# Optimization experiments

Measured on AMD Instinct MI355X. Metric: run time of the kernel, lower is better.

## Reference

```python
import jax, jax.numpy as jnp
import numpy as np

B, S = 1024, 64          # batch, num clips (att_size)
R = 1024                 # CG_rnn_size
E = 1024                 # CG_input_encoding_size
CD = 1024                # clip_context_dim
ED = 1024                # event_context_dim
H = 512                  # CG_att_hid_size


def setup_inputs() -> dict:
    key = jax.random.key(0)
    ks = jax.random.split(key, 20)
    s = 0.02
    return {
        "xt": jax.random.normal(ks[0], (B, E), jnp.float32),
        "video": jax.random.normal(ks[1], (B, 1024), jnp.float32),
        "event": jax.random.normal(ks[2], (B, ED), jnp.float32),
        "clip": jax.random.normal(ks[3], (B, S, CD), jnp.float32),
        "clip_mask": jax.random.randint(ks[4], (B, S), 0, 2, jnp.int32),
        "state_h": jax.random.normal(ks[5], (2, B, R), jnp.float32),
        "state_c": jax.random.normal(ks[6], (2, B, R), jnp.float32),
        # LSTMCell 0 (input = event ++ xt -> ED+E)
        "W_ih0": jax.random.normal(ks[7], (4 * R, ED + E), jnp.float32) * s,
        "b_ih0": jnp.zeros((4 * R,), jnp.float32),
        "W_hh0": jax.random.normal(ks[8], (4 * R, R), jnp.float32) * s,
        "b_hh0": jnp.zeros((4 * R,), jnp.float32),
        # LSTMCell 1 (input = att ++ xt -> CD+E)
        "W_ih1": jax.random.normal(ks[9], (4 * R, CD + E), jnp.float32) * s,
        "b_ih1": jnp.zeros((4 * R,), jnp.float32),
        "W_hh1": jax.random.normal(ks[10], (4 * R, R), jnp.float32) * s,
        "b_hh1": jnp.zeros((4 * R,), jnp.float32),
        # Attention params
        "W_ctx": jax.random.normal(ks[11], (H, CD), jnp.float32) * s,
        "b_ctx": jnp.zeros((H,), jnp.float32),
        "W_h2a": jax.random.normal(ks[12], (H, R), jnp.float32) * s,
        "b_h2a": jnp.zeros((H,), jnp.float32),
        "W_alpha": jax.random.normal(ks[13], (1, H), jnp.float32) * s,
        "b_alpha": jnp.zeros((1,), jnp.float32),
    }


def _lstm_cell(x, h, c, W_ih, b_ih, W_hh, b_hh):
    gates = x @ W_ih.T + b_ih + h @ W_hh.T + b_hh  # [B, 4R]
    i, f, g, o = jnp.split(gates, 4, axis=-1)
    i, f, o = jax.nn.sigmoid(i), jax.nn.sigmoid(f), jax.nn.sigmoid(o)
    g = jnp.tanh(g)
    c_new = f * c + i * g
    h_new = o * jnp.tanh(c_new)
    return h_new, c_new


def _attention(h, att_feats, att_mask, W_ctx, b_ctx, W_h2a, b_h2a, W_alpha, b_alpha):
    att = att_feats @ W_ctx.T + b_ctx                 # [B, S, H]
    att_h = h @ W_h2a.T + b_h2a                       # [B, H]
    dot = jnp.tanh(att + att_h[:, None, :])           # [B, S, H]
    scores = (dot @ W_alpha.T + b_alpha)[..., 0]      # [B, S]
    weight = jax.nn.softmax(scores, axis=1)
    m = att_mask.astype(weight.dtype)
    weight = weight * m
    weight = weight / jnp.sum(weight, axis=1, keepdims=True)
    return jnp.einsum('bs,bsd->bd', weight, att_feats)  # [B, CD]


def reference(xt, video, event, clip, clip_mask, state_h, state_c,
              W_ih0, b_ih0, W_hh0, b_hh0, W_ih1, b_ih1, W_hh1, b_hh1,
              W_ctx, b_ctx, W_h2a, b_h2a, W_alpha, b_alpha):
    pre_h1 = state_h[1]
    # stream 0: torch.cat((xt, event), 1)
    h0, c0 = _lstm_cell(jnp.concatenate([xt, event], axis=1),
                        state_h[0], state_c[0], W_ih0, b_ih0, W_hh0, b_hh0)
    att = _attention(pre_h1, clip, clip_mask,
                     W_ctx, b_ctx, W_h2a, b_h2a, W_alpha, b_alpha)
    h1, c1 = _lstm_cell(jnp.concatenate([xt, att], axis=1),
                        state_h[1], state_c[1], W_ih1, b_ih1, W_hh1, b_hh1)
    # dropout layers are identity in eval mode
    output = jnp.concatenate([h0, h1], axis=1)        # [B, 2R]
    new_h = jnp.stack([h0, h1])
    new_c = jnp.stack([c0, c1])
    return output, new_h, new_c
```

## Files before the change

kernel.cpp:

```cpp
#include <hip/hip_runtime.h>

typedef short short8 __attribute__((ext_vector_type(8)));
typedef float floatx4 __attribute__((ext_vector_type(4)));
typedef unsigned short u16;

__device__ __forceinline__ u16 cvt_bf(float x) {
  unsigned u = __float_as_uint(x);
  unsigned r = 0x7FFFu + ((u >> 16) & 1u);
  return (u16)((u + r) >> 16);
}
__device__ __forceinline__ float bf2f(u16 h) {
  return __uint_as_float(((unsigned)h) << 16);
}
__device__ __forceinline__ void gll16(const u16* g, u16* l) {
  __builtin_amdgcn_global_load_lds(
      (__attribute__((address_space(1))) void*)(void*)const_cast<u16*>(g),
      (__attribute__((address_space(3))) void*)(void*)l, 16, 0, 0);
}
__device__ __forceinline__ float fast_tanh(float x) {
  float t = __expf(-2.f * fabsf(x));
  float r = 1.f - 2.f * t / (1.f + t);
  return copysignf(r, x);
}
__device__ __forceinline__ float fast_sigm(float x) {
  return 1.f / (1.f + __expf(-x));
}

#define MAXSEG 9
struct ConvArgs {
  const float* src[MAXSEG];
  u16* dst[MAXSEG];
  unsigned lw[MAXSEG];
  unsigned dstride[MAXSEG];
  unsigned blk0[MAXSEG + 1];
  int nseg;
};
__global__ __launch_bounds__(256)
void convert_seg(ConvArgs a) {
  const unsigned blk = blockIdx.x;
  int s = 0;
  for (int i = 1; i < a.nseg; ++i) if (blk >= a.blk0[i]) s = i;
  const unsigned e0 = (blk - a.blk0[s]) * 2048u + threadIdx.x * 8u;
  const float* src = a.src[s] + e0;
  const float4 v0 = *(const float4*)src;
  const float4 v1 = *(const float4*)(src + 4);
  const unsigned row = e0 >> a.lw[s];
  const unsigned col = e0 & ((1u << a.lw[s]) - 1u);
  u16* d = a.dst[s] + (size_t)row * a.dstride[s] + col;
  short8 p;
  p[0] = (short)cvt_bf(v0.x); p[1] = (short)cvt_bf(v0.y);
  p[2] = (short)cvt_bf(v0.z); p[3] = (short)cvt_bf(v0.w);
  p[4] = (short)cvt_bf(v1.x); p[5] = (short)cvt_bf(v1.y);
  p[6] = (short)cvt_bf(v1.z); p[7] = (short)cvt_bf(v1.w);
  *(short8*)d = p;
}
__global__ __launch_bounds__(256)
void conv_flat(const float* __restrict__ src, u16* __restrict__ dst) {
  const size_t e = (size_t)blockIdx.x * 2048 + threadIdx.x * 8;
  const float4 v0 = *(const float4*)(src + e);
  const float4 v1 = *(const float4*)(src + e + 4);
  short8 p;
  p[0] = (short)cvt_bf(v0.x); p[1] = (short)cvt_bf(v0.y);
  p[2] = (short)cvt_bf(v0.z); p[3] = (short)cvt_bf(v0.w);
  p[4] = (short)cvt_bf(v1.x); p[5] = (short)cvt_bf(v1.y);
  p[6] = (short)cvt_bf(v1.z); p[7] = (short)cvt_bf(v1.w);
  *(short8*)(dst + e) = p;
}
__global__ __launch_bounds__(256)
void zerof(float* __restrict__ p) { p[blockIdx.x * 256 + threadIdx.x] = 0.f; }

template<int MODE>
__global__ __launch_bounds__(256, 3)
void gemm128(const u16* __restrict__ A, int sa, const u16* __restrict__ B, int sb,
             const float* __restrict__ bias0, const float* __restrict__ bias1,
             float* __restrict__ out, int N, int K,
             const float* __restrict__ atth, const float* __restrict__ Walpha,
             float* __restrict__ scores, int row0,
             const u16* A2, const u16* B2,
             const float* bias0b, const float* bias1b, float* out2)
{
  if (blockIdx.z) { A = A2; B = B2; bias0 = bias0b; bias1 = bias1b; out = out2; }
  __shared__ u16 sA[128 * 64];
  __shared__ u16 sB[128 * 64];

  const int tid = threadIdx.x, lane = tid & 63, w = tid >> 6;
  const int quad = lane >> 4, l15 = lane & 15;
  const int wm = w >> 1, wn = w & 1;
  const int Mbase = blockIdx.y * 128, Nbase = blockIdx.x * 128;
  const int srow = lane >> 3;
  const int sslot = (lane & 7) ^ srow;

  floatx4 acc[4][4] = {};

  for (int k0 = 0; k0 < K; k0 += 64) {
    __syncthreads();
#pragma unroll
    for (int j = 0; j < 4; ++j) {
      const int c = w + 4 * j;
      const int row = c * 8 + srow;
      gll16(A + (size_t)(Mbase + row) * sa + k0 + sslot * 8, &sA[c * 512]);
      gll16(B + (size_t)(Nbase + row) * sb + k0 + sslot * 8, &sB[c * 512]);
    }
    __syncthreads();
#pragma unroll
    for (int ks = 0; ks < 2; ++ks) {
      short8 af[4], bf[4];
#pragma unroll
      for (int mt = 0; mt < 4; ++mt) {
        const int row = wm * 64 + mt * 16 + l15;
        af[mt] = *(const short8*)&sA[row * 64 + ((ks * 4 + quad) ^ (row & 7)) * 8];
      }
#pragma unroll
      for (int nt = 0; nt < 4; ++nt) {
        const int row = wn * 64 + nt * 16 + l15;
        bf[nt] = *(const short8*)&sB[row * 64 + ((ks * 4 + quad) ^ (row & 7)) * 8];
      }
#pragma unroll
      for (int mt = 0; mt < 4; ++mt)
#pragma unroll
        for (int nt = 0; nt < 4; ++nt)
          acc[mt][nt] = __builtin_amdgcn_mfma_f32_16x16x32_bf16(af[mt], bf[nt], acc[mt][nt], 0, 0, 0);
    }
  }

  if (MODE == 0) {
#pragma unroll
    for (int nt = 0; nt < 4; ++nt) {
      const int col = Nbase + wn * 64 + nt * 16 + l15;
      const float bc = bias0[col] + bias1[col];
#pragma unroll
      for (int mt = 0; mt < 4; ++mt) {
        const int rb = Mbase + wm * 64 + mt * 16 + quad * 4;
#pragma unroll
        for (int r = 0; r < 4; ++r)
          out[(size_t)(rb + r) * N + col] = acc[mt][nt][r] + bc;
      }
    }
  } else {
    const int b = (row0 + Mbase + wm * 64) >> 6;
    float rs[4][4] = {};
#pragma unroll
    for (int nt = 0; nt < 4; ++nt) {
      const int col = Nbase + wn * 64 + nt * 16 + l15;
      const float wa = Walpha[col];
      const float ah = atth[(size_t)b * 512 + col];
#pragma unroll
      for (int mt = 0; mt < 4; ++mt)
#pragma unroll
        for (int r = 0; r < 4; ++r)
          rs[mt][r] += wa * fast_tanh(acc[mt][nt][r] + ah);
    }
#pragma unroll
    for (int mt = 0; mt < 4; ++mt)
#pragma unroll
      for (int r = 0; r < 4; ++r) {
        float v = rs[mt][r];
        v += __shfl_xor(v, 1); v += __shfl_xor(v, 2);
        v += __shfl_xor(v, 4); v += __shfl_xor(v, 8);
        if (l15 == 0)
          atomicAdd(&scores[row0 + Mbase + wm * 64 + mt * 16 + quad * 4 + r], v);
      }
  }
}

__global__ __launch_bounds__(256)
void softmax_k(const float* __restrict__ scores, const int* __restrict__ mask,
               float* __restrict__ wbuf)
{
  const int b = blockIdx.x * 4 + (threadIdx.x >> 6);
  const int s = threadIdx.x & 63;
  const float v = scores[b * 64 + s];
  float mx = v;
#pragma unroll
  for (int d = 32; d; d >>= 1) mx = fmaxf(mx, __shfl_xor(mx, d));
  const float e = __expf(v - mx) * (float)mask[b * 64 + s];
  float den = e;
#pragma unroll
  for (int d = 32; d; d >>= 1) den += __shfl_xor(den, d);
  wbuf[b * 64 + s] = e / den;
}

template<int BF>
__global__ __launch_bounds__(128)
void ctx_att(const float* __restrict__ clipf, const u16* __restrict__ clipb,
             const float* __restrict__ wbuf, u16* __restrict__ A1)
{
  __shared__ float w[64];
  const int b = blockIdx.x, tid = threadIdx.x;
  if (tid < 64) w[tid] = wbuf[b * 64 + tid];
  __syncthreads();
  const int c8 = tid * 8;
  float a[8] = {};
  if (BF) {
    const u16* base = clipb + (size_t)b * 65536 + c8;
#pragma unroll 4
    for (int s = 0; s < 64; ++s) {
      const float wt = w[s];
      const short8 c = *(const short8*)(base + (size_t)s * 1024);
#pragma unroll
      for (int j = 0; j < 8; ++j) a[j] += wt * bf2f((u16)c[j]);
    }
  } else {
    const float* base = clipf + (size_t)b * 65536 + c8;
#pragma unroll 4
    for (int s = 0; s < 64; ++s) {
      const float wt = w[s];
      const float4 v0 = *(const float4*)(base + (size_t)s * 1024);
      const float4 v1 = *(const float4*)(base + (size_t)s * 1024 + 4);
      a[0] += wt * v0.x; a[1] += wt * v0.y; a[2] += wt * v0.z; a[3] += wt * v0.w;
      a[4] += wt * v1.x; a[5] += wt * v1.y; a[6] += wt * v1.z; a[7] += wt * v1.w;
    }
  }
  short8 p;
#pragma unroll
  for (int j = 0; j < 8; ++j) p[j] = (short)cvt_bf(a[j]);
  *(short8*)&A1[(size_t)b * 3072 + 1024 + c8] = p;
}

__global__ __launch_bounds__(256)
void lstm_ew(const float* __restrict__ gates, const float* __restrict__ cprev,
             float* __restrict__ out, int st)
{
  const int idx = blockIdx.x * 256 + threadIdx.x;
  const int b = idx >> 8;
  const int r4 = (idx & 255) * 4;
  const float* g = gates + (size_t)b * 4096 + r4;
  const float4 gi = *(const float4*)g;
  const float4 gf = *(const float4*)(g + 1024);
  const float4 gg = *(const float4*)(g + 2048);
  const float4 go = *(const float4*)(g + 3072);
  const float4 c  = *(const float4*)(cprev + (size_t)b * 1024 + r4);
  float4 cn, hn;
  cn.x = fast_sigm(gf.x) * c.x + fast_sigm(gi.x) * fast_tanh(gg.x);  hn.x = fast_sigm(go.x) * fast_tanh(cn.x);
  cn.y = fast_sigm(gf.y) * c.y + fast_sigm(gi.y) * fast_tanh(gg.y);  hn.y = fast_sigm(go.y) * fast_tanh(cn.y);
  cn.z = fast_sigm(gf.z) * c.z + fast_sigm(gi.z) * fast_tanh(gg.z);  hn.z = fast_sigm(go.z) * fast_tanh(cn.z);
  cn.w = fast_sigm(gf.w) * c.w + fast_sigm(gi.w) * fast_tanh(gg.w);  hn.w = fast_sigm(go.w) * fast_tanh(cn.w);
  *(float4*)(out + (size_t)b * 2048 + st * 1024 + r4) = hn;
  *(float4*)(out + 2097152 + (size_t)st * 1048576 + (size_t)b * 1024 + r4) = hn;
  *(float4*)(out + 4194304 + (size_t)st * 1048576 + (size_t)b * 1024 + r4) = cn;
}

extern "C" void kernel_launch(void* const* d_in, const int* in_sizes, int n_in,
                              void* d_out, int out_size, void* d_ws, size_t ws_size,
                              hipStream_t stream) {
  (void)in_sizes; (void)n_in; (void)out_size;
  const float* xt      = (const float*)d_in[0];
  const float* event   = (const float*)d_in[2];
  const float* clip    = (const float*)d_in[3];
  const int*   cmask   = (const int*)d_in[4];
  const float* state_h = (const float*)d_in[5];
  const float* state_c = (const float*)d_in[6];
  const float* W_ih0   = (const float*)d_in[7];
  const float* b_ih0   = (const float*)d_in[8];
  const float* W_hh0   = (const float*)d_in[9];
  const float* b_hh0   = (const float*)d_in[10];
  const float* W_ih1   = (const float*)d_in[11];
  const float* b_ih1   = (const float*)d_in[12];
  const float* W_hh1   = (const float*)d_in[13];
  const float* b_hh1   = (const float*)d_in[14];
  const float* W_ctx   = (const float*)d_in[15];
  const float* b_ctx   = (const float*)d_in[16];
  const float* W_h2a   = (const float*)d_in[17];
  const float* b_h2a   = (const float*)d_in[18];
  const float* W_alpha = (const float*)d_in[19];

  int NC; bool grouped;
  if      (ws_size >= 207618048) { NC = 1; grouped = true;  }
  else if (ws_size >= 106954752) { NC = 4; grouped = true;  }
  else                           { NC = 8; grouped = false; }

  char* p = (char*)d_ws;
  float* gates0 = (float*)p; p += 16777216;
  float* gates1 = gates0;
  if (grouped) { gates1 = (float*)p; p += 16777216; }
  u16* A0 = (u16*)p; p += 6291456;
  u16* A1 = (u16*)p; p += 6291456;
  u16* W0 = (u16*)p; p += 25165824;
  u16* Wc = (u16*)p; p += 1048576;
  u16* Wh = (u16*)p; p += 1048576;
  u16* clipb = (u16*)p;
  u16* W1 = (u16*)p;
  float* atth   = gates0;
  float* wbuf   = gates0 + 524288;
  float* scores = gates0 + 589824;

  const float* h0p = state_h;
  const float* h1p = state_h + 1048576;
  const float* c0p = state_c;
  const float* c1p = state_c + 1048576;
  float* out = (float*)d_out;

  ConvArgs ca{};
  {
    const float* srcs[9] = {W_ctx, W_h2a, W_ih0, W_hh0, xt, event, h0p, xt, h1p};
    u16* dsts[9] = {Wc, Wh, W0, W0 + 2048, A0, A0 + 1024, A0 + 2048, A1, A1 + 2048};
    const unsigned lws[9]  = {10, 10, 11, 10, 10, 10, 10, 10, 10};
    const unsigned dstr[9] = {1024, 1024, 3072, 3072, 3072, 3072, 3072, 3072, 3072};
    const unsigned nblk[9] = {256, 256, 4096, 2048, 512, 512, 512, 512, 512};
    unsigned acc = 0;
    for (int i = 0; i < 9; ++i) {
      ca.src[i] = srcs[i]; ca.dst[i] = dsts[i];
      ca.lw[i] = lws[i]; ca.dstride[i] = dstr[i];
      ca.blk0[i] = acc; acc += nblk[i];
    }
    ca.blk0[9] = acc; ca.nseg = 9;
    convert_seg<<<acc, 256, 0, stream>>>(ca);
  }

  zerof<<<256, 256, 0, stream>>>(scores);

  gemm128<0><<<dim3(4, 8, 1), 256, 0, stream>>>(
      A1 + 2048, 3072, Wh, 1024, b_h2a, b_ctx, atth, 512, 1024,
      nullptr, nullptr, nullptr, 0, nullptr, nullptr, nullptr, nullptr, nullptr);

  const int rows = 65536 / NC;
  for (int c = 0; c < NC; ++c) {
    conv_flat<<<rows * 1024 / 2048, 256, 0, stream>>>(clip + (size_t)c * rows * 1024, clipb);
    gemm128<1><<<dim3(4, rows / 128, 1), 256, 0, stream>>>(
        clipb, 1024, Wc, 1024, nullptr, nullptr, nullptr, 512, 1024,
        atth, W_alpha, scores, c * rows,
        nullptr, nullptr, nullptr, nullptr, nullptr);
  }

  softmax_k<<<256, 256, 0, stream>>>(scores, cmask, wbuf);

  if (NC == 1) ctx_att<1><<<1024, 128, 0, stream>>>(clip, clipb, wbuf, A1);
  else         ctx_att<0><<<1024, 128, 0, stream>>>(clip, clipb, wbuf, A1);

  ConvArgs cb{};
  {
    const float* srcs[2] = {W_ih1, W_hh1};
    u16* dsts[2] = {W1, W1 + 2048};
    const unsigned lws[2] = {11, 10};
    const unsigned nblk[2] = {4096, 2048};
    unsigned acc = 0;
    for (int i = 0; i < 2; ++i) {
      cb.src[i] = srcs[i]; cb.dst[i] = dsts[i];
      cb.lw[i] = lws[i]; cb.dstride[i] = 3072;
      cb.blk0[i] = acc; acc += nblk[i];
    }
    cb.blk0[2] = acc; cb.nseg = 2;
    convert_seg<<<acc, 256, 0, stream>>>(cb);
  }

  if (grouped) {
    gemm128<0><<<dim3(32, 8, 2), 256, 0, stream>>>(
        A0, 3072, W0, 3072, b_ih0, b_hh0, gates0, 4096, 3072,
        nullptr, nullptr, nullptr, 0,
        A1, W1, b_ih1, b_hh1, gates1);
    lstm_ew<<<1024, 256, 0, stream>>>(gates0, c0p, out, 0);
    lstm_ew<<<1024, 256, 0, stream>>>(gates1, c1p, out, 1);
  } else {
    gemm128<0><<<dim3(32, 8, 1), 256, 0, stream>>>(
        A0, 3072, W0, 3072, b_ih0, b_hh0, gates0, 4096, 3072,
        nullptr, nullptr, nullptr, 0, nullptr, nullptr, nullptr, nullptr, nullptr);
    lstm_ew<<<1024, 256, 0, stream>>>(gates0, c0p, out, 0);
    gemm128<0><<<dim3(32, 8, 1), 256, 0, stream>>>(
        A1, 3072, W1, 3072, b_ih1, b_hh1, gates0, 4096, 3072,
        nullptr, nullptr, nullptr, 0, nullptr, nullptr, nullptr, nullptr, nullptr);
    lstm_ew<<<1024, 256, 0, stream>>>(gates0, c1p, out, 1);
  }
}
```

Before: 710.4 us.

## Add large-workspace path fusing GEMMs and elementwise stages into fewer launches

With enough workspace, a new path converts all weights and the full clip tensor to bf16 at once. It then fuses independent work into shared launches: the h2a GEMM runs alongside the clip conversion, the LSTM0 GEMM alongside the attention-score GEMM, and the LSTM1 GEMM (split-K in two halves) alongside the LSTM0 elementwise step. Score zeroing is folded into the conversion kernel through a null-source segment. Softmax and the context reduction are merged into one kernel that reads the bf16 clip. This cuts launch count and per-chunk serialization, at the cost of extra workspace and an extra pass to sum the split-K partial gates.

Result: faster. 680.3 us (-4.2%).

```diff
diff --git a/kernel.cpp b/kernel.cpp
--- a/kernel.cpp
+++ b/kernel.cpp
@@ -26,7 +26,7 @@
   return 1.f / (1.f + __expf(-x));
 }
 
-#define MAXSEG 9
+#define MAXSEG 13
 struct ConvArgs {
   const float* src[MAXSEG];
   u16* dst[MAXSEG];
@@ -41,17 +41,22 @@
   int s = 0;
   for (int i = 1; i < a.nseg; ++i) if (blk >= a.blk0[i]) s = i;
   const unsigned e0 = (blk - a.blk0[s]) * 2048u + threadIdx.x * 8u;
-  const float* src = a.src[s] + e0;
-  const float4 v0 = *(const float4*)src;
-  const float4 v1 = *(const float4*)(src + 4);
-  const unsigned row = e0 >> a.lw[s];
-  const unsigned col = e0 & ((1u << a.lw[s]) - 1u);
-  u16* d = a.dst[s] + (size_t)row * a.dstride[s] + col;
-  short8 p;
-  p[0] = (short)cvt_bf(v0.x); p[1] = (short)cvt_bf(v0.y);
-  p[2] = (short)cvt_bf(v0.z); p[3] = (short)cvt_bf(v0.w);
-  p[4] = (short)cvt_bf(v1.x); p[5] = (short)cvt_bf(v1.y);
-  p[6] = (short)cvt_bf(v1.z); p[7] = (short)cvt_bf(v1.w);
+  short8 p = {};
+  u16* d;
+  const float* src = a.src[s];
+  if (src) {
+    const float4 v0 = *(const float4*)(src + e0);
+    const float4 v1 = *(const float4*)(src + e0 + 4);
+    const unsigned row = e0 >> a.lw[s];
+    const unsigned col = e0 & ((1u << a.lw[s]) - 1u);
+    d = a.dst[s] + (size_t)row * a.dstride[s] + col;
+    p[0] = (short)cvt_bf(v0.x); p[1] = (short)cvt_bf(v0.y);
+    p[2] = (short)cvt_bf(v0.z); p[3] = (short)cvt_bf(v0.w);
+    p[4] = (short)cvt_bf(v1.x); p[5] = (short)cvt_bf(v1.y);
+    p[6] = (short)cvt_bf(v1.z); p[7] = (short)cvt_bf(v1.w);
+  } else {
+    d = a.dst[s] + e0;
+  }
   *(short8*)d = p;
 }
 __global__ __launch_bounds__(256)
@@ -69,6 +74,137 @@
 __global__ __launch_bounds__(256)
 void zerof(float* __restrict__ p) { p[blockIdx.x * 256 + threadIdx.x] = 0.f; }
 
+__device__ __forceinline__ void gemm_body(
+    const u16* __restrict__ A, int sa, const u16* __restrict__ B, int sb,
+    int K, int Mbase, int Nbase, u16* sA, u16* sB, floatx4 (&acc)[4][4])
+{
+  const int tid = threadIdx.x, lane = tid & 63, w = tid >> 6;
+  const int quad = lane >> 4, l15 = lane & 15;
+  const int wm = w >> 1, wn = w & 1;
+  const int srow = lane >> 3;
+  const int sslot = (lane & 7) ^ srow;
+
+  for (int k0 = 0; k0 < K; k0 += 64) {
+    __syncthreads();
+#pragma unroll
+    for (int j = 0; j < 4; ++j) {
+      const int c = w + 4 * j;
+      const int row = c * 8 + srow;
+      gll16(A + (size_t)(Mbase + row) * sa + k0 + sslot * 8, &sA[c * 512]);
+      gll16(B + (size_t)(Nbase + row) * sb + k0 + sslot * 8, &sB[c * 512]);
+    }
+    __syncthreads();
+#pragma unroll
+    for (int ks = 0; ks < 2; ++ks) {
+      short8 af[4], bf[4];
+#pragma unroll
+      for (int mt = 0; mt < 4; ++mt) {
+        const int row = wm * 64 + mt * 16 + l15;
+        af[mt] = *(const short8*)&sA[row * 64 + ((ks * 4 + quad) ^ (row & 7)) * 8];
+      }
+#pragma unroll
+      for (int nt = 0; nt < 4; ++nt) {
+        const int row = wn * 64 + nt * 16 + l15;
+        bf[nt] = *(const short8*)&sB[row * 64 + ((ks * 4 + quad) ^ (row & 7)) * 8];
+      }
+#pragma unroll
+      for (int mt = 0; mt < 4; ++mt)
+#pragma unroll
+        for (int nt = 0; nt < 4; ++nt)
+          acc[mt][nt] = __builtin_amdgcn_mfma_f32_16x16x32_bf16(af[mt], bf[nt], acc[mt][nt], 0, 0, 0);
+    }
+  }
+}
+
+__device__ __forceinline__ void epi_store(
+    floatx4 (&acc)[4][4], const float* __restrict__ bias0,
+    const float* __restrict__ bias1, float* __restrict__ out,
+    int N, int Mbase, int Nbase)
+{
+  const int tid = threadIdx.x, lane = tid & 63, w = tid >> 6;
+  const int quad = lane >> 4, l15 = lane & 15;
+  const int wm = w >> 1, wn = w & 1;
+#pragma unroll
+  for (int nt = 0; nt < 4; ++nt) {
+    const int col = Nbase + wn * 64 + nt * 16 + l15;
+    const float bc = bias0 ? (bias0[col] + bias1[col]) : 0.f;
+#pragma unroll
+    for (int mt = 0; mt < 4; ++mt) {
+      const int rb = Mbase + wm * 64 + mt * 16 + quad * 4;
+#pragma unroll
+      for (int r = 0; r < 4; ++r)
+        out[(size_t)(rb + r) * N + col] = acc[mt][nt][r] + bc;
+    }
+  }
+}
+
+__device__ __forceinline__ void epi_score(
+    floatx4 (&acc)[4][4], const float* __restrict__ atth,
+    const float* __restrict__ Walpha, float* __restrict__ scores,
+    int Mbase, int Nbase)
+{
+  const int tid = threadIdx.x, lane = tid & 63, w = tid >> 6;
+  const int quad = lane >> 4, l15 = lane & 15;
+  const int wm = w >> 1, wn = w & 1;
+  const int b = (Mbase + wm * 64) >> 6;
+  float rs[4][4] = {};
+#pragma unroll
+  for (int nt = 0; nt < 4; ++nt) {
+    const int col = Nbase + wn * 64 + nt * 16 + l15;
+    const float wa = Walpha[col];
+    const float ah = atth[(size_t)b * 512 + col];
+#pragma unroll
+    for (int mt = 0; mt < 4; ++mt)
+#pragma unroll
+      for (int r = 0; r < 4; ++r)
+        rs[mt][r] += wa * fast_tanh(acc[mt][nt][r] + ah);
+  }
+#pragma unroll
+  for (int mt = 0; mt < 4; ++mt)
+#pragma unroll
+    for (int r = 0; r < 4; ++r) {
+      float v = rs[mt][r];
+      v += __shfl_xor(v, 1); v += __shfl_xor(v, 2);
+      v += __shfl_xor(v, 4); v += __shfl_xor(v, 8);
+      if (l15 == 0)
+        atomicAdd(&scores[Mbase + wm * 64 + mt * 16 + quad * 4 + r], v);
+    }
+}
+
+__device__ __forceinline__ void lstm_body(
+    const float* __restrict__ gates, const float* __restrict__ g1b,
+    const float* __restrict__ cprev, float* __restrict__ out, int st, int blk)
+{
+  const int idx = blk * 256 + (int)threadIdx.x;
+  const int b = idx >> 8;
+  const int r4 = (idx & 255) * 4;
+  const float* g = gates + (size_t)b * 4096 + r4;
+  float4 gi = *(const float4*)g;
+  float4 gf = *(const float4*)(g + 1024);
+  float4 gg = *(const float4*)(g + 2048);
+  float4 go = *(const float4*)(g + 3072);
+  if (g1b) {
+    const float* h = g1b + (size_t)b * 4096 + r4;
+    const float4 hi = *(const float4*)h;
+    const float4 hf = *(const float4*)(h + 1024);
+    const float4 hg = *(const float4*)(h + 2048);
+    const float4 ho = *(const float4*)(h + 3072);
+    gi.x += hi.x; gi.y += hi.y; gi.z += hi.z; gi.w += hi.w;
+    gf.x += hf.x; gf.y += hf.y; gf.z += hf.z; gf.w += hf.w;
+    gg.x += hg.x; gg.y += hg.y; gg.z += hg.z; gg.w += hg.w;
+    go.x += ho.x; go.y += ho.y; go.z += ho.z; go.w += ho.w;
+  }
+  const float4 c = *(const float4*)(cprev + (size_t)b * 1024 + r4);
+  float4 cn, hn;
+  cn.x = fast_sigm(gf.x) * c.x + fast_sigm(gi.x) * fast_tanh(gg.x);  hn.x = fast_sigm(go.x) * fast_tanh(cn.x);
+  cn.y = fast_sigm(gf.y) * c.y + fast_sigm(gi.y) * fast_tanh(gg.y);  hn.y = fast_sigm(go.y) * fast_tanh(cn.y);
+  cn.z = fast_sigm(gf.z) * c.z + fast_sigm(gi.z) * fast_tanh(gg.z);  hn.z = fast_sigm(go.z) * fast_tanh(cn.z);
+  cn.w = fast_sigm(gf.w) * c.w + fast_sigm(gi.w) * fast_tanh(gg.w);  hn.w = fast_sigm(go.w) * fast_tanh(cn.w);
+  *(float4*)(out + (size_t)b * 2048 + st * 1024 + r4) = hn;
+  *(float4*)(out + 2097152 + (size_t)st * 1048576 + (size_t)b * 1024 + r4) = hn;
+  *(float4*)(out + 4194304 + (size_t)st * 1048576 + (size_t)b * 1024 + r4) = cn;
+}
+
 template<int MODE>
 __global__ __launch_bounds__(256, 3)
 void gemm128(const u16* __restrict__ A, int sa, const u16* __restrict__ B, int sb,
@@ -82,85 +218,11 @@
   if (blockIdx.z) { A = A2; B = B2; bias0 = bias0b; bias1 = bias1b; out = out2; }
   __shared__ u16 sA[128 * 64];
   __shared__ u16 sB[128 * 64];
-
-  const int tid = threadIdx.x, lane = tid & 63, w = tid >> 6;
-  const int quad = lane >> 4, l15 = lane & 15;
-  const int wm = w >> 1, wn = w & 1;
   const int Mbase = blockIdx.y * 128, Nbase = blockIdx.x * 128;
-  const int srow = lane >> 3;
-  const int sslot = (lane & 7) ^ srow;
-
   floatx4 acc[4][4] = {};
-
-  for (int k0 = 0; k0 < K; k0 += 64) {
-    __syncthreads();
-#pragma unroll
-    for (int j = 0; j < 4; ++j) {
-      const int c = w + 4 * j;
-      const int row = c * 8 + srow;
-      gll16(A + (size_t)(Mbase + row) * sa + k0 + sslot * 8, &sA[c * 512]);
-      gll16(B + (size_t)(Nbase + row) * sb + k0 + sslot * 8, &sB[c * 512]);
-    }
-    __syncthreads();
-#pragma unroll
-    for (int ks = 0; ks < 2; ++ks) {
-      short8 af[4], bf[4];
-#pragma unroll
-      for (int mt = 0; mt < 4; ++mt) {
-        const int row = wm * 64 + mt * 16 + l15;
-        af[mt] = *(const short8*)&sA[row * 64 + ((ks * 4 + quad) ^ (row & 7)) * 8];
-      }
-#pragma unroll
-      for (int nt = 0; nt < 4; ++nt) {
-        const int row = wn * 64 + nt * 16 + l15;
-        bf[nt] = *(const short8*)&sB[row * 64 + ((ks * 4 + quad) ^ (row & 7)) * 8];
-      }
-#pragma unroll
-      for (int mt = 0; mt < 4; ++mt)
-#pragma unroll
-        for (int nt = 0; nt < 4; ++nt)
-          acc[mt][nt] = __builtin_amdgcn_mfma_f32_16x16x32_bf16(af[mt], bf[nt], acc[mt][nt], 0, 0, 0);
-    }
-  }
-
-  if (MODE == 0) {
-#pragma unroll
-    for (int nt = 0; nt < 4; ++nt) {
-      const int col = Nbase + wn * 64 + nt * 16 + l15;
-      const float bc = bias0[col] + bias1[col];
-#pragma unroll
-      for (int mt = 0; mt < 4; ++mt) {
-        const int rb = Mbase + wm * 64 + mt * 16 + quad * 4;
-#pragma unroll
-        for (int r = 0; r < 4; ++r)
-          out[(size_t)(rb + r) * N + col] = acc[mt][nt][r] + bc;
-      }
-    }
-  } else {
-    const int b = (row0 + Mbase + wm * 64) >> 6;
-    float rs[4][4] = {};
-#pragma unroll
-    for (int nt = 0; nt < 4; ++nt) {
-      const int col = Nbase + wn * 64 + nt * 16 + l15;
-      const float wa = Walpha[col];
-      const float ah = atth[(size_t)b * 512 + col];
-#pragma unroll
-      for (int mt = 0; mt < 4; ++mt)
-#pragma unroll
-        for (int r = 0; r < 4; ++r)
-          rs[mt][r] += wa * fast_tanh(acc[mt][nt][r] + ah);
-    }
-#pragma unroll
-    for (int mt = 0; mt < 4; ++mt)
-#pragma unroll
-      for (int r = 0; r < 4; ++r) {
-        float v = rs[mt][r];
-        v += __shfl_xor(v, 1); v += __shfl_xor(v, 2);
-        v += __shfl_xor(v, 4); v += __shfl_xor(v, 8);
-        if (l15 == 0)
-          atomicAdd(&scores[row0 + Mbase + wm * 64 + mt * 16 + quad * 4 + r], v);
-      }
-  }
+  gemm_body(A, sa, B, sb, K, Mbase, Nbase, sA, sB, acc);
+  if (MODE == 0) epi_store(acc, bias0, bias1, out, N, Mbase, Nbase);
+  else           epi_score(acc, atth, Walpha, scores, row0 + Mbase, Nbase);
 }
 
 __global__ __launch_bounds__(256)
@@ -221,23 +283,123 @@
 void lstm_ew(const float* __restrict__ gates, const float* __restrict__ cprev,
              float* __restrict__ out, int st)
 {
-  const int idx = blockIdx.x * 256 + threadIdx.x;
-  const int b = idx >> 8;
-  const int r4 = (idx & 255) * 4;
-  const float* g = gates + (size_t)b * 4096 + r4;
-  const float4 gi = *(const float4*)g;
-  const float4 gf = *(const float4*)(g + 1024);
-  const float4 gg = *(const float4*)(g + 2048);
-  const float4 go = *(const float4*)(g + 3072);
-  const float4 c  = *(const float4*)(cprev + (size_t)b * 1024 + r4);
-  float4 cn, hn;
-  cn.x = fast_sigm(gf.x) * c.x + fast_sigm(gi.x) * fast_tanh(gg.x);  hn.x = fast_sigm(go.x) * fast_tanh(cn.x);
-  cn.y = fast_sigm(gf.y) * c.y + fast_sigm(gi.y) * fast_tanh(gg.y);  hn.y = fast_sigm(go.y) * fast_tanh(cn.y);
-  cn.z = fast_sigm(gf.z) * c.z + fast_sigm(gi.z) * fast_tanh(gg.z);  hn.z = fast_sigm(go.z) * fast_tanh(cn.z);
-  cn.w = fast_sigm(gf.w) * c.w + fast_sigm(gi.w) * fast_tanh(gg.w);  hn.w = fast_sigm(go.w) * fast_tanh(cn.w);
-  *(float4*)(out + (size_t)b * 2048 + st * 1024 + r4) = hn;
-  *(float4*)(out + 2097152 + (size_t)st * 1048576 + (size_t)b * 1024 + r4) = hn;
-  *(float4*)(out + 4194304 + (size_t)st * 1048576 + (size_t)b * 1024 + r4) = cn;
+  lstm_body(gates, nullptr, cprev, out, st, blockIdx.x);
+}
+
+__global__ __launch_bounds__(256, 3)
+void conv_atth(const float* __restrict__ clip, u16* __restrict__ clipb,
+               const u16* __restrict__ A1, const u16* __restrict__ Wh,
+               const float* __restrict__ b_h2a, const float* __restrict__ b_ctx,
+               float* __restrict__ atth)
+{
+  __shared__ u16 sA[128 * 64];
+  __shared__ u16 sB[128 * 64];
+  const int bid = blockIdx.x;
+  if (bid < 32) {
+    const int Nbase = (bid & 3) * 128, Mbase = (bid >> 2) * 128;
+    floatx4 acc[4][4] = {};
+    gemm_body(A1 + 2048, 3072, Wh, 1024, 1024, Mbase, Nbase, sA, sB, acc);
+    epi_store(acc, b_h2a, b_ctx, atth, 512, Mbase, Nbase);
+    return;
+  }
+  const size_t e = (size_t)(bid - 32) * 2048 + threadIdx.x * 8;
+  const float4 v0 = *(const float4*)(clip + e);
+  const float4 v1 = *(const float4*)(clip + e + 4);
+  short8 p;
+  p[0] = (short)cvt_bf(v0.x); p[1] = (short)cvt_bf(v0.y);
+  p[2] = (short)cvt_bf(v0.z); p[3] = (short)cvt_bf(v0.w);
+  p[4] = (short)cvt_bf(v1.x); p[5] = (short)cvt_bf(v1.y);
+  p[6] = (short)cvt_bf(v1.z); p[7] = (short)cvt_bf(v1.w);
+  *(short8*)(clipb + e) = p;
+}
+
+__global__ __launch_bounds__(256, 3)
+void g0score(const u16* __restrict__ A0, const u16* __restrict__ W0,
+             const float* __restrict__ bi0, const float* __restrict__ bh0,
+             float* __restrict__ gates0,
+             const u16* __restrict__ clipb, const u16* __restrict__ Wc,
+             const float* __restrict__ atth, const float* __restrict__ Walpha,
+             float* __restrict__ scores)
+{
+  __shared__ u16 sA[128 * 64];
+  __shared__ u16 sB[128 * 64];
+  floatx4 acc[4][4] = {};
+  const int bid = blockIdx.x;
+  if (bid < 256) {
+    const int Nbase = (bid & 31) * 128, Mbase = (bid >> 5) * 128;
+    gemm_body(A0, 3072, W0, 3072, 3072, Mbase, Nbase, sA, sB, acc);
+    epi_store(acc, bi0, bh0, gates0, 4096, Mbase, Nbase);
+  } else {
+    const int t = bid - 256;
+    const int Nbase = (t & 3) * 128, Mbase = (t >> 2) * 128;
+    gemm_body(clipb, 1024, Wc, 1024, 1024, Mbase, Nbase, sA, sB, acc);
+    epi_score(acc, atth, Walpha, scores, Mbase, Nbase);
+  }
+}
+
+__global__ __launch_bounds__(128)
+void sm_ctx(const float* __restrict__ scores, const int* __restrict__ cmask,
+            const u16* __restrict__ clipb, u16* __restrict__ A1)
+{
+  __shared__ float w[64];
+  const int b = blockIdx.x, tid = threadIdx.x;
+  if (tid < 64) {
+    const float v = scores[b * 64 + tid];
+    float mx = v;
+#pragma unroll
+    for (int d = 32; d; d >>= 1) mx = fmaxf(mx, __shfl_xor(mx, d));
+    const float e = __expf(v - mx) * (float)cmask[b * 64 + tid];
+    float den = e;
+#pragma unroll
+    for (int d = 32; d; d >>= 1) den += __shfl_xor(den, d);
+    w[tid] = e / den;
+  }
+  __syncthreads();
+  const int c8 = tid * 8;
+  float a[8] = {};
+  const u16* base = clipb + (size_t)b * 65536 + c8;
+#pragma unroll 4
+  for (int s = 0; s < 64; ++s) {
+    const float wt = w[s];
+    const short8 c = *(const short8*)(base + (size_t)s * 1024);
+#pragma unroll
+    for (int j = 0; j < 8; ++j) a[j] += wt * bf2f((u16)c[j]);
+  }
+  short8 p;
+#pragma unroll
+  for (int j = 0; j < 8; ++j) p[j] = (short)cvt_bf(a[j]);
+  *(short8*)&A1[(size_t)b * 3072 + 1024 + c8] = p;
+}
+
+__global__ __launch_bounds__(256, 3)
+void g1ew(const u16* __restrict__ A1, const u16* __restrict__ W1,
+          const float* __restrict__ bi1, const float* __restrict__ bh1,
+          float* __restrict__ g1a, float* __restrict__ g1b,
+          const float* __restrict__ gates0, const float* __restrict__ c0p,
+          float* __restrict__ out)
+{
+  __shared__ u16 sA[128 * 64];
+  __shared__ u16 sB[128 * 64];
+  const int bid = blockIdx.x;
+  if (bid < 512) {
+    floatx4 acc[4][4] = {};
+    const int half = bid >> 8;
+    const int t = bid & 255;
+    const int Nbase = (t & 31) * 128, Mbase = (t >> 5) * 128;
+    const int k0 = half * 1536;
+    gemm_body(A1 + k0, 3072, W1 + k0, 3072, 1536, Mbase, Nbase, sA, sB, acc);
+    if (half == 0) epi_store(acc, bi1, bh1, g1a, 4096, Mbase, Nbase);
+    else           epi_store(acc, nullptr, nullptr, g1b, 4096, Mbase, Nbase);
+  } else {
+    lstm_body(gates0, nullptr, c0p, out, 0, bid - 512);
+  }
+}
+
+__global__ __launch_bounds__(256)
+void ew1sum(const float* __restrict__ g1a, const float* __restrict__ g1b,
+            const float* __restrict__ c1p, float* __restrict__ out)
+{
+  lstm_body(g1a, g1b, c1p, out, 1, blockIdx.x);
 }
 
 extern "C" void kernel_launch(void* const* d_in, const int* in_sizes, int n_in,
@@ -264,6 +426,62 @@
   const float* b_h2a   = (const float*)d_in[18];
   const float* W_alpha = (const float*)d_in[19];
 
+  const float* h0p = state_h;
+  const float* h1p = state_h + 1048576;
+  const float* c0p = state_c;
+  const float* c1p = state_c + 1048576;
+  float* out = (float*)d_out;
+
+  if (ws_size >= 251920384) {
+    char* p = (char*)d_ws;
+    float* gates0 = (float*)p; p += 16777216;
+    float* g1a    = (float*)p; p += 16777216;
+    float* g1b    = (float*)p; p += 16777216;
+    u16* A0 = (u16*)p; p += 6291456;
+    u16* A1 = (u16*)p; p += 6291456;
+    u16* W0 = (u16*)p; p += 25165824;
+    u16* W1 = (u16*)p; p += 25165824;
+    u16* Wc = (u16*)p; p += 1048576;
+    u16* Wh = (u16*)p; p += 1048576;
+    u16* clipb = (u16*)p; p += 134217728;
+    float* atth   = (float*)p; p += 2097152;
+    float* scores = (float*)p;
+
+    ConvArgs ca{};
+    {
+      const float* srcs[12] = {W_ctx, W_h2a, W_ih0, W_hh0, W_ih1, W_hh1,
+                               xt, event, h0p, xt, h1p, nullptr};
+      u16* dsts[12] = {Wc, Wh, W0, W0 + 2048, W1, W1 + 2048,
+                       A0, A0 + 1024, A0 + 2048, A1, A1 + 2048, (u16*)scores};
+      const unsigned lws[12]  = {10, 10, 11, 10, 11, 10, 10, 10, 10, 10, 10, 17};
+      const unsigned dstr[12] = {1024, 1024, 3072, 3072, 3072, 3072,
+                                 3072, 3072, 3072, 3072, 3072, 0};
+      const unsigned nblk[12] = {256, 256, 4096, 2048, 4096, 2048,
+                                 512, 512, 512, 512, 512, 64};
+      unsigned acc = 0;
+      for (int i = 0; i < 12; ++i) {
+        ca.src[i] = srcs[i]; ca.dst[i] = dsts[i];
+        ca.lw[i] = lws[i]; ca.dstride[i] = dstr[i];
+        ca.blk0[i] = acc; acc += nblk[i];
+      }
+      ca.blk0[12] = acc; ca.nseg = 12;
+      convert_seg<<<acc, 256, 0, stream>>>(ca);
+    }
+
+    conv_atth<<<32800, 256, 0, stream>>>(clip, clipb, A1, Wh, b_h2a, b_ctx, atth);
+
+    g0score<<<2304, 256, 0, stream>>>(A0, W0, b_ih0, b_hh0, gates0,
+                                      clipb, Wc, atth, W_alpha, scores);
+
+    sm_ctx<<<1024, 128, 0, stream>>>(scores, cmask, clipb, A1);
+
+    g1ew<<<1536, 256, 0, stream>>>(A1, W1, b_ih1, b_hh1, g1a, g1b,
+                                   gates0, c0p, out);
+
+    ew1sum<<<1024, 256, 0, stream>>>(g1a, g1b, c1p, out);
+    return;
+  }
+
   int NC; bool grouped;
   if      (ws_size >= 207618048) { NC = 1; grouped = true;  }
   else if (ws_size >= 106954752) { NC = 4; grouped = true;  }
@@ -283,12 +501,6 @@
   float* atth   = gates0;
   float* wbuf   = gates0 + 524288;
   float* scores = gates0 + 589824;
-
-  const float* h0p = state_h;
-  const float* h1p = state_h + 1048576;
-  const float* c0p = state_c;
-  const float* c1p = state_c + 1048576;
-  float* out = (float*)d_out;
 
   ConvArgs ca{};
   {
```
